# Kernel optimization log

Measured on AMD Instinct MI355X. Metric: run time of the kernel, lower is better.

## Reference

```python
import jax, jax.numpy as jnp
import numpy as np

D_MODEL = 64
D_STATE = 16
D_CONV = 4
EXPAND = 2
D_INNER = EXPAND * D_MODEL        # 128
DT_RANK = max(1, D_MODEL // 16)   # 4 (mamba_ssm default ceil(d_model/16))
BATCH, HH, WW = 2, 128, 128


def setup_inputs() -> dict:
    key = jax.random.key(0)
    ks = jax.random.split(key, 10)
    def norm(k, shape, sc=0.05):
        return jax.random.normal(k, shape, jnp.float32) * sc
    # A initialized as in mamba_ssm: A = 1..d_state per channel, stored as log
    A_log = jnp.log(jnp.tile(jnp.arange(1, D_STATE + 1, dtype=jnp.float32), (4, D_INNER, 1)))
    return {
        "x": jax.random.normal(ks[0], (BATCH, D_MODEL, HH, WW), jnp.float32),
        "in_w": norm(ks[1], (4, 2 * D_INNER, D_MODEL)),
        "conv_w": norm(ks[2], (4, D_INNER, D_CONV), 0.2),
        "conv_b": jnp.zeros((4, D_INNER), jnp.float32),
        "xp_w": norm(ks[3], (4, DT_RANK + 2 * D_STATE, D_INNER)),
        "dtp_w": norm(ks[4], (4, D_INNER, DT_RANK), 0.2),
        "dtp_b": jnp.full((4, D_INNER), -4.0, jnp.float32) + norm(ks[5], (4, D_INNER), 0.5),
        "A_log": A_log,
        "Dp": jnp.ones((4, D_INNER), jnp.float32),
        "out_w": norm(ks[6], (4, D_MODEL, D_INNER)),
        "fuse_w": norm(ks[7], (D_MODEL, 4 * D_MODEL)),
        "fuse_b": jnp.zeros((D_MODEL,), jnp.float32),
        "ln_g": jnp.ones((D_MODEL,), jnp.float32),
        "ln_b": jnp.zeros((D_MODEL,), jnp.float32),
    }


def _mamba(xseq, in_w, conv_w, conv_b, xp_w, dtp_w, dtp_b, A_log, Dp, out_w):
    # xseq: (N, L, d_model) -> (N, L, d_model). Single-direction Mamba block.
    N, L, _ = xseq.shape
    xz = xseq @ in_w.T                       # (N, L, 2*d_inner)
    u, z = jnp.split(xz, 2, axis=-1)
    # causal depthwise conv1d, kernel width D_CONV
    up = jnp.pad(u, ((0, 0), (D_CONV - 1, 0), (0, 0)))
    uc = conv_b + sum(up[:, k:k + L, :] * conv_w[:, k][None, None, :] for k in range(D_CONV))
    uc = jax.nn.silu(uc)
    dbl = uc @ xp_w.T                        # (N, L, dt_rank + 2*d_state)
    dt = jax.nn.softplus(dbl[..., :DT_RANK] @ dtp_w.T + dtp_b)   # (N, L, d_inner)
    Bm = dbl[..., DT_RANK:DT_RANK + D_STATE]                     # (N, L, d_state)
    Cm = dbl[..., DT_RANK + D_STATE:]                            # (N, L, d_state)
    A = -jnp.exp(A_log)                                          # (d_inner, d_state)

    def step(h, inp):
        dt_t, B_t, C_t, u_t = inp            # (N,d_inner),(N,d_state),(N,d_state),(N,d_inner)
        h = h * jnp.exp(dt_t[..., None] * A) + (dt_t * u_t)[..., None] * B_t[:, None, :]
        y = jnp.einsum('nds,ns->nd', h, C_t)
        return h, y

    h0 = jnp.zeros((N, D_INNER, D_STATE), xseq.dtype)
    _, ys = jax.lax.scan(step, h0, (dt.swapaxes(0, 1), Bm.swapaxes(0, 1),
                                    Cm.swapaxes(0, 1), uc.swapaxes(0, 1)))
    y = ys.swapaxes(0, 1) + uc * Dp
    y = y * jax.nn.silu(z)
    return y @ out_w.T


def reference(x, in_w, conv_w, conv_b, xp_w, dtp_w, dtp_b, A_log, Dp, out_w,
              fuse_w, fuse_b, ln_g, ln_b):
    B, C, H, W = x.shape
    xhwc = x.transpose(0, 2, 3, 1)           # (B,H,W,C)
    xwhc = x.transpose(0, 3, 2, 1)           # (B,W,H,C)
    d0 = xhwc.reshape(B * H, W, C)                         # horizontal fwd
    d1 = xhwc[:, :, ::-1, :].reshape(B * H, W, C)          # horizontal bwd
    d2 = xwhc.reshape(B * W, H, C)                         # vertical fwd
    d3 = xwhc[:, :, ::-1, :].reshape(B * W, H, C)          # vertical bwd
    xd = jnp.stack([d0, d1, d2, d3])         # (4, B*S, S, C) since H == W
    ys = jax.vmap(_mamba)(xd, in_w, conv_w, conv_b, xp_w, dtp_w, dtp_b, A_log, Dp, out_w)
    y0 = ys[0].reshape(B, H, W, C)
    y1 = ys[1].reshape(B, H, W, C)[:, :, ::-1, :]
    y2 = ys[2].reshape(B, W, H, C).transpose(0, 2, 1, 3)
    y3 = ys[3].reshape(B, W, H, C)[:, :, ::-1, :].transpose(0, 2, 1, 3)
    cat = jnp.concatenate([y0, y1, y2, y3], axis=-1)       # (B,H,W,4C)
    f = cat @ fuse_w.T + fuse_b                            # 1x1 conv
    mu = f.mean(-1, keepdims=True)
    var = f.var(-1, keepdims=True)
    f = (f - mu) * jax.lax.rsqrt(var + 1e-5) * ln_g + ln_b # LayerNorm over C
    f = jax.nn.silu(f)
    return f.transpose(0, 3, 1, 2)                          # (B,C,H,W)
```

## Files before the change

### kernel.cpp

```cpp
#include <hip/hip_runtime.h>
#include <hip/hip_bf16.h>
#include <math.h>


typedef __attribute__((ext_vector_type(8))) short short8;
typedef __attribute__((ext_vector_type(4))) float f32x4;
typedef __attribute__((ext_vector_type(2))) float f32x2;

__device__ __forceinline__ f32x2 pk_mul(f32x2 a, f32x2 b) {
  f32x2 d;
  asm("v_pk_mul_f32 %0, %1, %2" : "=v"(d) : "v"(a), "v"(b));
  return d;
}
__device__ __forceinline__ f32x2 pk_fma(f32x2 a, f32x2 b, f32x2 c) {
  f32x2 d;
  asm("v_pk_fma_f32 %0, %1, %2, %3" : "=v"(d) : "v"(a), "v"(b), "v"(c));
  return d;
}

__device__ __forceinline__ unsigned int pk2bf(float a, float b) {
  __hip_bfloat162 h = __float22bfloat162_rn(make_float2(a, b));
  unsigned int u;
  __builtin_memcpy(&u, &h, 4);
  return u;
}
__device__ __forceinline__ unsigned short f2bf(float f) {
  __hip_bfloat16 h = __float2bfloat16(f);
  unsigned short s;
  __builtin_memcpy(&s, &h, 2);
  return s;
}
__device__ __forceinline__ float bf2f(unsigned short h) {
  return __uint_as_float(((unsigned int)h) << 16);
}
__device__ __forceinline__ float fastrcp(float x) { return __builtin_amdgcn_rcpf(x); }
__device__ __forceinline__ float siluf(float x) { return x * fastrcp(1.f + __expf(-x)); }

__global__ void k0_prep(const float* __restrict__ out_w, const float* __restrict__ fuse_w,
                        const float* __restrict__ in_w, const float* __restrict__ xp_w,
                        const float* __restrict__ x,
                        unsigned short* __restrict__ MT16, unsigned short* __restrict__ W16,
                        unsigned short* __restrict__ XW16, unsigned short* __restrict__ XH,
                        unsigned short* __restrict__ XW) {
  __shared__ unsigned short sT[64*132];
  int blk = blockIdx.x;
  int tid = threadIdx.x;
  if (blk < 128) {
    int idx = blk * 256 + tid;
    int d   = idx & 127;
    int o   = (idx >> 7) & 63;
    int dir = idx >> 13;
    float acc = 0.f;
    #pragma unroll 8
    for (int j = 0; j < 64; ++j)
      acc += out_w[(dir*64 + j)*128 + d] * fuse_w[o*256 + dir*64 + j];
    MT16[o*512 + dir*128 + d] = f2bf(acc);
  } else if (blk < 160) {
    int t = (blk - 128) * 256 + tid;
    int base = t * 8;
    float4 v0 = *(const float4*)(in_w + base);
    float4 v1 = *(const float4*)(in_w + base + 4);
    uint4 pk;
    pk.x = pk2bf(v0.x, v0.y);
    pk.y = pk2bf(v0.z, v0.w);
    pk.z = pk2bf(v1.x, v1.y);
    pk.w = pk2bf(v1.z, v1.w);
    *(uint4*)(W16 + base) = pk;
  } else if (blk < 164) {
    int t = (blk - 160) * 256 + tid;
    for (int pid = t; pid < 4*48*128; pid += 1024) {
      int dir = pid / 6144;
      int rem = pid - dir*6144;
      int row = rem >> 7, c = rem & 127;
      XW16[pid] = (row < 36) ? f2bf(xp_w[dir*4608 + row*128 + c]) : (unsigned short)0;
    }
  } else {
    int idx = blk - 164;
    int b = idx >> 7, h = idx & 127;
    for (int f = tid*4; f < 8192; f += 1024) {
      int c = f >> 7, w = f & 127;
      float4 v = *(const float4*)(x + (((size_t)(b*64 + c)*128 + h)*128 + w));
      sT[c*132 + w + 0] = f2bf(v.x);
      sT[c*132 + w + 1] = f2bf(v.y);
      sT[c*132 + w + 2] = f2bf(v.z);
      sT[c*132 + w + 3] = f2bf(v.w);
    }
    __syncthreads();
    for (int f = tid*8; f < 8192; f += 2048) {
      int w = f >> 6, c0 = f & 63;
      unsigned int pk[4];
      #pragma unroll
      for (int p = 0; p < 4; ++p) {
        unsigned int lo = sT[(c0 + p*2 + 0)*132 + w];
        unsigned int hi = sT[(c0 + p*2 + 1)*132 + w];
        pk[p] = lo | (hi << 16);
      }
      uint4 v; v.x = pk[0]; v.y = pk[1]; v.z = pk[2]; v.w = pk[3];
      *(uint4*)(XH + (((size_t)(b*128 + h)*128 + w)*64 + c0)) = v;
      *(uint4*)(XW + (((size_t)(b*128 + w)*128 + h)*64 + c0)) = v;
    }
  }
}

__global__ __launch_bounds__(256, 3) void k1_front(
    const unsigned short* __restrict__ XH, const unsigned short* __restrict__ XW,
    const unsigned short* __restrict__ W16, const unsigned short* __restrict__ XW16,
    const float* __restrict__ conv_w, const float* __restrict__ conv_b,
    const float* __restrict__ dtp_w, const float* __restrict__ dtp_b,
    const float* __restrict__ A_log, const float* __restrict__ Dp,
    unsigned short* __restrict__ YF)
{
  __shared__ __align__(16) char smem[53248];
  float* sBCf         = (float*)smem;
  unsigned short* sUC = (unsigned short*)(smem + 18432);

  const int tid = threadIdx.x;
  const int dir = blockIdx.x >> 8;
  const int n   = blockIdx.x & 255;
  const int b   = n >> 7;
  const int r   = n & 127;
  const int n_all = dir*256 + n;

  const unsigned short* xsrc = (dir < 2 ? XH : XW) + ((size_t)(b*128 + r)*128)*64;

  const int wave = tid >> 6;
  const int lane = tid & 63;
  const int m16 = lane & 15;
  const int quad = lane >> 4;
  const int tb0 = wave * 32;
  const int st0 = tb0 + m16;
  const int st1 = tb0 + 16 + m16;
  const int sp0 = (dir & 1) ? (127 - st0) : st0;
  const int sp1 = (dir & 1) ? (127 - st1) : st1;

  unsigned int zpk[2][8][2];

  {
    short8 bfr[2][2];
    #pragma unroll
    for (int ks = 0; ks < 2; ++ks) {
      bfr[0][ks] = *(const short8*)(xsrc + sp0*64 + ks*32 + quad*8);
      bfr[1][ks] = *(const short8*)(xsrc + sp1*64 + ks*32 + quad*8);
    }
    const unsigned short* Wd = W16 + (size_t)dir * 16384;

    for (int rt = 0; rt < 8; ++rt) {
      short8 af[2];
      #pragma unroll
      for (int ks = 0; ks < 2; ++ks)
        af[ks] = *(const short8*)(Wd + (rt*16 + m16)*64 + ks*32 + quad*8);
      #pragma unroll
      for (int tt = 0; tt < 2; ++tt) {
        f32x4 acc = {0.f, 0.f, 0.f, 0.f};
        acc = __builtin_amdgcn_mfma_f32_16x16x32_bf16(af[0], bfr[tt][0], acc, 0, 0, 0);
        acc = __builtin_amdgcn_mfma_f32_16x16x32_bf16(af[1], bfr[tt][1], acc, 0, 0, 0);
        const int tok = tt ? st1 : st0;
        const int r0 = rt*16 + quad*4;
        uint2 u2;
        u2.x = pk2bf(acc[0], acc[1]);
        u2.y = pk2bf(acc[2], acc[3]);
        *(uint2*)(sUC + tok*136 + r0) = u2;
      }
    }
    #pragma unroll
    for (int k = 0; k < 8; ++k) {
      short8 af[2];
      #pragma unroll
      for (int ks = 0; ks < 2; ++ks)
        af[ks] = *(const short8*)(Wd + ((8+k)*16 + m16)*64 + ks*32 + quad*8);
      #pragma unroll
      for (int tt = 0; tt < 2; ++tt) {
        f32x4 acc = {0.f, 0.f, 0.f, 0.f};
        acc = __builtin_amdgcn_mfma_f32_16x16x32_bf16(af[0], bfr[tt][0], acc, 0, 0, 0);
        acc = __builtin_amdgcn_mfma_f32_16x16x32_bf16(af[1], bfr[tt][1], acc, 0, 0, 0);
        zpk[tt][k][0] = pk2bf(siluf(acc[0]), siluf(acc[1]));
        zpk[tt][k][1] = pk2bf(siluf(acc[2]), siluf(acc[3]));
      }
    }
  }
  __syncthreads();

  {
    const int d = tid & 127;
    const int half = tid >> 7;
    const int ca = half * 32;
    const int cb2 = (half + 2) * 32;
    const float* cw = conv_w + (size_t)(dir*128 + d)*4;
    const float c0w = cw[0], c1w = cw[1], c2w = cw[2], c3w = cw[3];
    const float cbv = conv_b[dir*128 + d];
    const f32x2 cw0v = {c0w, c0w}, cw1v = {c1w, c1w}, cw2v = {c2w, c2w}, cw3v = {c3w, c3w};
    const f32x2 cbv2 = {cbv, cbv};
    f32x2 A0 = { half ? bf2f(sUC[(ca-3)*136 + d]) : 0.f, bf2f(sUC[(cb2-3)*136 + d]) };
    f32x2 A1 = { half ? bf2f(sUC[(ca-2)*136 + d]) : 0.f, bf2f(sUC[(cb2-2)*136 + d]) };
    f32x2 A2 = { half ? bf2f(sUC[(ca-1)*136 + d]) : 0.f, bf2f(sUC[(cb2-1)*136 + d]) };
    __syncthreads();
    unsigned short* pa = sUC + ca*136 + d;
    unsigned short* pb = sUC + cb2*136 + d;
    for (int i = 0; i < 32; ++i) {
      f32x2 cur = { bf2f(*pa), bf2f(*pb) };
      f32x2 v = pk_fma(cw3v, cur,
                pk_fma(cw2v, A2,
                pk_fma(cw1v, A1,
                pk_fma(cw0v, A0, cbv2))));
      *pa = f2bf(siluf(v.x));
      *pb = f2bf(siluf(v.y));
      A0 = A1; A1 = A2; A2 = cur;
      pa += 136; pb += 136;
    }
  }
  __syncthreads();

  {
    short8 bfr[2][4];
    #pragma unroll
    for (int tt = 0; tt < 2; ++tt)
      #pragma unroll
      for (int ks = 0; ks < 4; ++ks)
        bfr[tt][ks] = *(const short8*)(sUC + (tt ? st1 : st0)*136 + ks*32 + quad*8);

    const unsigned short* XWd = XW16 + (size_t)dir * (48*128);

    for (int rt = 0; rt < 3; ++rt) {
      short8 af[4];
      #pragma unroll
      for (int ks = 0; ks < 4; ++ks)
        af[ks] = *(const short8*)(XWd + (rt*16 + m16)*128 + ks*32 + quad*8);
      #pragma unroll
      for (int tt = 0; tt < 2; ++tt) {
        f32x4 acc = {0.f, 0.f, 0.f, 0.f};
        #pragma unroll
        for (int ks = 0; ks < 4; ++ks)
          acc = __builtin_amdgcn_mfma_f32_16x16x32_bf16(af[ks], bfr[tt][ks], acc, 0, 0, 0);
        const int tok = tt ? st1 : st0;
        const int r0 = rt*16 + quad*4;
        if (r0 == 0) {
          float4 v; v.x = acc[0]; v.y = acc[1]; v.z = acc[2]; v.w = acc[3];
          *(float4*)(smem + 18432 + tok*272 + 256) = v;
        } else if (r0 < 36) {
          float4 v; v.x = acc[0]; v.y = acc[1]; v.z = acc[2]; v.w = acc[3];
          *(float4*)(sBCf + tok*36 + (r0 - 4)) = v;
        }
      }
    }
  }
  __syncthreads();

  {
    const int d = tid >> 1;
    const int p = tid & 1;
    const float* dwp = dtp_w + (size_t)(dir*128 + d) * 4;
    const float dw0 = dwp[0], dw1 = dwp[1], dw2 = dwp[2], dw3 = dwp[3];
    const float db = dtp_b[dir*128 + d];
    const float dpv = Dp[dir*128 + d];

    float Av[8];
    bool fast = true;
    #pragma unroll
    for (int j = 0; j < 8; ++j) {
      float a = -__expf(A_log[((size_t)(dir*128 + d))*16 + p*8 + j]);
      Av[j] = a;
      if (fabsf((-a) - (float)(p*8 + j + 1)) > 1e-3f) fast = false;
    }

    if (fast) {
      f32x2 h0 = {0.f, 0.f}, h1 = {0.f, 0.f}, h2v = {0.f, 0.f}, h3 = {0.f, 0.f};
      const char* qp = smem + 18432 + 256;
      const float* bp = sBCf + p*8;
      const float* cp = sBCf + 16 + p*8;
      const unsigned short* up = sUC + d;
      unsigned short* yo = sUC + d;
      for (int l = 0; l < 128; ++l) {
        float4 Q = *(const float4*)qp;
        f32x2 B01 = *(const f32x2*)(bp + 0), B23 = *(const f32x2*)(bp + 2);
        f32x2 B45 = *(const f32x2*)(bp + 4), B67 = *(const f32x2*)(bp + 6);
        f32x2 C01 = *(const f32x2*)(cp + 0), C23 = *(const f32x2*)(cp + 2);
        f32x2 C45 = *(const f32x2*)(cp + 4), C67 = *(const f32x2*)(cp + 6);
        float u = bf2f(*up);
        float dr = Q.x*dw0 + Q.y*dw1 + Q.z*dw2 + Q.w*dw3 + db;
        float te = __expf(dr);
        float dt = (dr > 20.f) ? dr : __logf(1.f + te);
        float dtu = dt * u;
        float E = fastrcp(1.f + te);
        float E2 = E*E, E4 = E2*E2, E8 = E4*E4;
        float eb = p ? E8 : 1.f;
        f32x2 P0 = {E*eb, E2*eb};
        f32x2 E2v = {E2, E2};
        f32x2 P1 = pk_mul(P0, E2v);
        f32x2 P2 = pk_mul(P1, E2v);
        f32x2 P3 = pk_mul(P2, E2v);
        f32x2 du = {dtu, dtu};
        h0  = pk_fma(h0,  P0, pk_mul(du, B01));
        h1  = pk_fma(h1,  P1, pk_mul(du, B23));
        h2v = pk_fma(h2v, P2, pk_mul(du, B45));
        h3  = pk_fma(h3,  P3, pk_mul(du, B67));
        f32x2 ya = pk_mul(h0, C01);
        f32x2 yb = pk_mul(h1, C23);
        ya = pk_fma(h2v, C45, ya);
        yb = pk_fma(h3,  C67, yb);
        float ypar = (ya.x + ya.y) + (yb.x + yb.y);
        float ot = __uint_as_float((unsigned int)__builtin_amdgcn_mov_dpp(
                     (int)__float_as_uint(ypar), 0xB1, 0xF, 0xF, true));
        float ysum = ypar + ot;
        *yo = f2bf(ysum + u*dpv);
        qp += 272; bp += 36; cp += 36; up += 136; yo += 136;
      }
    } else {
      float h[8];
      #pragma unroll
      for (int j = 0; j < 8; ++j) h[j] = 0.f;
      for (int l = 0; l < 128; ++l) {
        float4 Q = *(const float4*)(smem + 18432 + l*272 + 256);
        float4 b0 = *(const float4*)(sBCf + l*36 + p*8);
        float4 b1 = *(const float4*)(sBCf + l*36 + p*8 + 4);
        float4 c0 = *(const float4*)(sBCf + l*36 + 16 + p*8);
        float4 c1 = *(const float4*)(sBCf + l*36 + 16 + p*8 + 4);
        float Bv[8] = {b0.x,b0.y,b0.z,b0.w, b1.x,b1.y,b1.z,b1.w};
        float Cv[8] = {c0.x,c0.y,c0.z,c0.w, c1.x,c1.y,c1.z,c1.w};
        float u = bf2f(sUC[l*136 + d]);
        float dr = Q.x*dw0 + Q.y*dw1 + Q.z*dw2 + Q.w*dw3 + db;
        float te = __expf(dr);
        float dt = (dr > 20.f) ? dr : __logf(1.f + te);
        float dtu = dt * u;
        float yp = 0.f;
        #pragma unroll
        for (int j = 0; j < 8; ++j) {
          float ej = __expf(dt*Av[j]);
          h[j] = h[j]*ej + dtu*Bv[j];
          yp += h[j]*Cv[j];
        }
        float ot = __uint_as_float((unsigned int)__builtin_amdgcn_mov_dpp(
                     (int)__float_as_uint(yp), 0xB1, 0xF, 0xF, true));
        float ysum = yp + ot;
        if (p == 0) sUC[l*136 + d] = f2bf(ysum + u*dpv);
      }
    }
  }
  __syncthreads();

  #pragma unroll
  for (int tt = 0; tt < 2; ++tt) {
    const int st = tt ? st1 : st0;
    size_t rowbase;
    if (dir < 2)       rowbase = ((size_t)n_all*128 + st)*128;
    else if (dir == 2) rowbase = ((size_t)(512 + b*128 + st)*128 + r)*128;
    else               rowbase = ((size_t)(768 + b*128 + (127-st))*128 + r)*128;
    #pragma unroll
    for (int k = 0; k < 8; ++k) {
      const int dz = 16*k + quad*4;
      uint2 yv = *(const uint2*)(sUC + st*136 + dz);
      float y0 = __uint_as_float(yv.x << 16);
      float y1 = __uint_as_float(yv.x & 0xffff0000u);
      float y2 = __uint_as_float(yv.y << 16);
      float y3 = __uint_as_float(yv.y & 0xffff0000u);
      unsigned int z01 = zpk[tt][k][0], z23 = zpk[tt][k][1];
      float z0 = __uint_as_float(z01 << 16);
      float z1 = __uint_as_float(z01 & 0xffff0000u);
      float z2 = __uint_as_float(z23 << 16);
      float z3 = __uint_as_float(z23 & 0xffff0000u);
      uint2 ov;
      ov.x = pk2bf(y0*z0, y1*z1);
      ov.y = pk2bf(y2*z2, y3*z3);
      *(uint2*)(YF + rowbase + dz) = ov;
    }
  }
}

__global__ __launch_bounds__(256, 2) void k3_fuse(
    const unsigned short* __restrict__ YF, const unsigned short* __restrict__ MT16,
    const float* __restrict__ fuse_b, const float* __restrict__ ln_g,
    const float* __restrict__ ln_b, float* __restrict__ out)
{
  __shared__ __align__(16) unsigned short sYB[64*520];

  const int tid = threadIdx.x;
  const int blk = blockIdx.x;
  const int b = blk >> 8;
  const int rr2 = blk & 255;
  const int h = rr2 >> 1;
  const int w0 = (rr2 & 1) * 64;

  for (int f = tid*8; f < 32768; f += 2048) {
    int dirg = f >> 13;
    int rem = f & 8191;
    int tok = rem >> 7;
    int dd = rem & 127;
    int X = (dirg == 1) ? (127 - w0 - tok) : (w0 + tok);
    size_t base = ((size_t)(dirg*256 + b*128 + h)*128 + X)*128 + dd;
    *(uint4*)(sYB + tok*520 + dirg*128 + dd) = *(const uint4*)(YF + base);
  }
  __syncthreads();

  const int wave = tid >> 6;
  const int lane = tid & 63;
  const int m16 = lane & 15;
  const int quad = lane >> 4;
  const int tok = wave*16 + m16;

  short8 bfr[16];
  #pragma unroll
  for (int jt = 0; jt < 16; ++jt)
    bfr[jt] = *(const short8*)(sYB + tok*520 + jt*32 + quad*8);

  float facc[4][4];
  #pragma unroll
  for (int mt = 0; mt < 4; ++mt) {
    f32x4 acc = {0.f, 0.f, 0.f, 0.f};
    #pragma unroll
    for (int jt = 0; jt < 16; ++jt) {
      short8 af = *(const short8*)(MT16 + (size_t)(mt*16 + m16)*512 + jt*32 + quad*8);
      acc = __builtin_amdgcn_mfma_f32_16x16x32_bf16(af, bfr[jt], acc, 0, 0, 0);
    }
    facc[mt][0] = acc[0]; facc[mt][1] = acc[1]; facc[mt][2] = acc[2]; facc[mt][3] = acc[3];
  }

  float fv[16];
  float s1 = 0.f, s2 = 0.f;
  #pragma unroll
  for (int mt = 0; mt < 4; ++mt)
    #pragma unroll
    for (int rr = 0; rr < 4; ++rr) {
      int o = mt*16 + quad*4 + rr;
      float v = facc[mt][rr] + fuse_b[o];
      fv[mt*4 + rr] = v;
      s1 += v; s2 += v*v;
    }
  s1 += __shfl_xor(s1, 16, 64); s1 += __shfl_xor(s1, 32, 64);
  s2 += __shfl_xor(s2, 16, 64); s2 += __shfl_xor(s2, 32, 64);
  float mu = s1 * (1.f/64.f);
  float var = s2 * (1.f/64.f) - mu*mu;
  float rs = rsqrtf(var + 1e-5f);

  #pragma unroll
  for (int mt = 0; mt < 4; ++mt)
    #pragma unroll
    for (int rr = 0; rr < 4; ++rr) {
      int o = mt*16 + quad*4 + rr;
      float v = (fv[mt*4 + rr] - mu) * rs * ln_g[o] + ln_b[o];
      out[((size_t)(b*64 + o)*128 + h)*128 + (w0 + tok)] = siluf(v);
    }
}

extern "C" void kernel_launch(void* const* d_in, const int* in_sizes, int n_in,
                              void* d_out, int out_size, void* d_ws, size_t ws_size,
                              hipStream_t stream) {
  const float* x      = (const float*)d_in[0];
  const float* in_w   = (const float*)d_in[1];
  const float* conv_w = (const float*)d_in[2];
  const float* conv_b = (const float*)d_in[3];
  const float* xp_w   = (const float*)d_in[4];
  const float* dtp_w  = (const float*)d_in[5];
  const float* dtp_b  = (const float*)d_in[6];
  const float* A_log  = (const float*)d_in[7];
  const float* Dp     = (const float*)d_in[8];
  const float* out_w  = (const float*)d_in[9];
  const float* fuse_w = (const float*)d_in[10];
  const float* fuse_b = (const float*)d_in[11];
  const float* ln_g   = (const float*)d_in[12];
  const float* ln_b   = (const float*)d_in[13];
  float* out = (float*)d_out;

  char* ws = (char*)d_ws;
  unsigned short* YF   = (unsigned short*)(ws);
  unsigned short* MT16 = (unsigned short*)(ws + 33554432);
  unsigned short* W16  = (unsigned short*)(ws + 33619968);
  unsigned short* XW16 = (unsigned short*)(ws + 33751040);
  unsigned short* XH   = (unsigned short*)(ws + 33800192);
  unsigned short* XWt  = (unsigned short*)(ws + 37994496);

  k0_prep<<<dim3(420), dim3(256), 0, stream>>>(out_w, fuse_w, in_w, xp_w, x,
                                               MT16, W16, XW16, XH, XWt);
  k1_front<<<dim3(1024), dim3(256), 0, stream>>>(XH, XWt, W16, XW16, conv_w, conv_b,
                                                 dtp_w, dtp_b, A_log, Dp, YF);
  k3_fuse<<<dim3(512), dim3(256), 0, stream>>>(YF, MT16, fuse_b, ln_g, ln_b, out);
}
```

Before: 205.0 us.

## Split front kernel into projection/conv kernel and separate global-memory scan kernel

After: 272.8 us. 33.0% more time.

```diff
diff --git a/kernel.cpp b/kernel.cpp
--- a/kernel.cpp
+++ b/kernel.cpp
@@ -102,17 +102,14 @@
   }
 }
 
-__global__ __launch_bounds__(256, 3) void k1_front(
+__global__ __launch_bounds__(256, 4) void k1a_front(
     const unsigned short* __restrict__ XH, const unsigned short* __restrict__ XW,
     const unsigned short* __restrict__ W16, const unsigned short* __restrict__ XW16,
     const float* __restrict__ conv_w, const float* __restrict__ conv_b,
-    const float* __restrict__ dtp_w, const float* __restrict__ dtp_b,
-    const float* __restrict__ A_log, const float* __restrict__ Dp,
-    unsigned short* __restrict__ YF)
+    unsigned short* __restrict__ UCg, unsigned short* __restrict__ ZFg,
+    float* __restrict__ BCg)
 {
-  __shared__ __align__(16) char smem[53248];
-  float* sBCf         = (float*)smem;
-  unsigned short* sUC = (unsigned short*)(smem + 18432);
+  __shared__ __align__(16) unsigned short sUC[128*136];
 
   const int tid = threadIdx.x;
   const int dir = blockIdx.x >> 8;
@@ -132,8 +129,6 @@
   const int st1 = tb0 + 16 + m16;
   const int sp0 = (dir & 1) ? (127 - st0) : st0;
   const int sp1 = (dir & 1) ? (127 - st1) : st1;
-
-  unsigned int zpk[2][8][2];
 
   {
     short8 bfr[2][2];
@@ -162,6 +157,7 @@
         *(uint2*)(sUC + tok*136 + r0) = u2;
       }
     }
+    unsigned short* zn = ZFg + (size_t)n_all * 16384;
     #pragma unroll
     for (int k = 0; k < 8; ++k) {
       short8 af[2];
@@ -173,8 +169,11 @@
         f32x4 acc = {0.f, 0.f, 0.f, 0.f};
         acc = __builtin_amdgcn_mfma_f32_16x16x32_bf16(af[0], bfr[tt][0], acc, 0, 0, 0);
         acc = __builtin_amdgcn_mfma_f32_16x16x32_bf16(af[1], bfr[tt][1], acc, 0, 0, 0);
-        zpk[tt][k][0] = pk2bf(siluf(acc[0]), siluf(acc[1]));
-        zpk[tt][k][1] = pk2bf(siluf(acc[2]), siluf(acc[3]));
+        const int tok = tt ? st1 : st0;
+        uint2 zv;
+        zv.x = pk2bf(siluf(acc[0]), siluf(acc[1]));
+        zv.y = pk2bf(siluf(acc[2]), siluf(acc[3]));
+        *(uint2*)(zn + tok*128 + 16*k + quad*4) = zv;
       }
     }
   }
@@ -211,6 +210,14 @@
   __syncthreads();
 
   {
+    unsigned short* ucn = UCg + (size_t)n_all * 16384;
+    #pragma unroll
+    for (int c = 0; c < 8; ++c) {
+      int idx = tid + c*256;
+      int tok = idx >> 4, u4 = idx & 15;
+      *(uint4*)(ucn + tok*128 + u4*8) = *(const uint4*)(sUC + tok*136 + u4*8);
+    }
+
     short8 bfr[2][4];
     #pragma unroll
     for (int tt = 0; tt < 2; ++tt)
@@ -219,6 +226,7 @@
         bfr[tt][ks] = *(const short8*)(sUC + (tt ? st1 : st0)*136 + ks*32 + quad*8);
 
     const unsigned short* XWd = XW16 + (size_t)dir * (48*128);
+    float* bcn = BCg + (size_t)n_all * 4608;
 
     for (int rt = 0; rt < 3; ++rt) {
       short8 af[4];
@@ -232,135 +240,146 @@
         for (int ks = 0; ks < 4; ++ks)
           acc = __builtin_amdgcn_mfma_f32_16x16x32_bf16(af[ks], bfr[tt][ks], acc, 0, 0, 0);
         const int tok = tt ? st1 : st0;
-        const int r0 = rt*16 + quad*4;
-        if (r0 == 0) {
+        const int g = rt*4 + quad;
+        if (g < 9) {
           float4 v; v.x = acc[0]; v.y = acc[1]; v.z = acc[2]; v.w = acc[3];
-          *(float4*)(smem + 18432 + tok*272 + 256) = v;
-        } else if (r0 < 36) {
-          float4 v; v.x = acc[0]; v.y = acc[1]; v.z = acc[2]; v.w = acc[3];
-          *(float4*)(sBCf + tok*36 + (r0 - 4)) = v;
+          *(float4*)(bcn + g*512 + tok*4) = v;
         }
       }
     }
   }
-  __syncthreads();
-
-  {
-    const int d = tid >> 1;
-    const int p = tid & 1;
-    const float* dwp = dtp_w + (size_t)(dir*128 + d) * 4;
-    const float dw0 = dwp[0], dw1 = dwp[1], dw2 = dwp[2], dw3 = dwp[3];
-    const float db = dtp_b[dir*128 + d];
-    const float dpv = Dp[dir*128 + d];
-
-    float Av[8];
-    bool fast = true;
-    #pragma unroll
-    for (int j = 0; j < 8; ++j) {
-      float a = -__expf(A_log[((size_t)(dir*128 + d))*16 + p*8 + j]);
-      Av[j] = a;
-      if (fabsf((-a) - (float)(p*8 + j + 1)) > 1e-3f) fast = false;
-    }
-
-    if (fast) {
-      f32x2 h0 = {0.f, 0.f}, h1 = {0.f, 0.f}, h2v = {0.f, 0.f}, h3 = {0.f, 0.f};
-      const char* qp = smem + 18432 + 256;
-      const float* bp = sBCf + p*8;
-      const float* cp = sBCf + 16 + p*8;
-      const unsigned short* up = sUC + d;
-      unsigned short* yo = sUC + d;
-      for (int l = 0; l < 128; ++l) {
-        float4 Q = *(const float4*)qp;
-        f32x2 B01 = *(const f32x2*)(bp + 0), B23 = *(const f32x2*)(bp + 2);
-        f32x2 B45 = *(const f32x2*)(bp + 4), B67 = *(const f32x2*)(bp + 6);
-        f32x2 C01 = *(const f32x2*)(cp + 0), C23 = *(const f32x2*)(cp + 2);
-        f32x2 C45 = *(const f32x2*)(cp + 4), C67 = *(const f32x2*)(cp + 6);
-        float u = bf2f(*up);
-        float dr = Q.x*dw0 + Q.y*dw1 + Q.z*dw2 + Q.w*dw3 + db;
-        float te = __expf(dr);
-        float dt = (dr > 20.f) ? dr : __logf(1.f + te);
-        float dtu = dt * u;
-        float E = fastrcp(1.f + te);
-        float E2 = E*E, E4 = E2*E2, E8 = E4*E4;
-        float eb = p ? E8 : 1.f;
-        f32x2 P0 = {E*eb, E2*eb};
-        f32x2 E2v = {E2, E2};
-        f32x2 P1 = pk_mul(P0, E2v);
-        f32x2 P2 = pk_mul(P1, E2v);
-        f32x2 P3 = pk_mul(P2, E2v);
-        f32x2 du = {dtu, dtu};
-        h0  = pk_fma(h0,  P0, pk_mul(du, B01));
-        h1  = pk_fma(h1,  P1, pk_mul(du, B23));
-        h2v = pk_fma(h2v, P2, pk_mul(du, B45));
-        h3  = pk_fma(h3,  P3, pk_mul(du, B67));
-        f32x2 ya = pk_mul(h0, C01);
-        f32x2 yb = pk_mul(h1, C23);
-        ya = pk_fma(h2v, C45, ya);
-        yb = pk_fma(h3,  C67, yb);
-        float ypar = (ya.x + ya.y) + (yb.x + yb.y);
-        float ot = __uint_as_float((unsigned int)__builtin_amdgcn_mov_dpp(
-                     (int)__float_as_uint(ypar), 0xB1, 0xF, 0xF, true));
-        float ysum = ypar + ot;
-        *yo = f2bf(ysum + u*dpv);
-        qp += 272; bp += 36; cp += 36; up += 136; yo += 136;
+}
+
+__global__ __launch_bounds__(256, 4) void k1b_scan(
+    const unsigned short* __restrict__ UCg, const unsigned short* __restrict__ ZFg,
+    const float* __restrict__ BCg,
+    const float* __restrict__ dtp_w, const float* __restrict__ dtp_b,
+    const float* __restrict__ A_log, const float* __restrict__ Dp,
+    unsigned short* __restrict__ YF)
+{
+  const int tid = threadIdx.x;
+  const int dir = blockIdx.x >> 8;
+  const int n   = blockIdx.x & 255;
+  const int b   = n >> 7;
+  const int r   = n & 127;
+  const int n_all = dir*256 + n;
+  const int d = tid >> 1;
+  const int p = tid & 1;
+
+  const float* dwp = dtp_w + (size_t)(dir*128 + d) * 4;
+  const float dw0 = dwp[0], dw1 = dwp[1], dw2 = dwp[2], dw3 = dwp[3];
+  const float db = dtp_b[dir*128 + d];
+  const float dpv = Dp[dir*128 + d];
+
+  float Av[8];
+  bool fast = true;
+  #pragma unroll
+  for (int j = 0; j < 8; ++j) {
+    float a = -__expf(A_log[((size_t)(dir*128 + d))*16 + p*8 + j]);
+    Av[j] = a;
+    if (fabsf((-a) - (float)(p*8 + j + 1)) > 1e-3f) fast = false;
+  }
+
+  const float* bcn = BCg + (size_t)n_all * 4608;
+  const float* qp  = bcn;
+  const float* bp0 = bcn + (1 + 2*p)*512;
+  const float* bp1 = bcn + (2 + 2*p)*512;
+  const float* cp0 = bcn + (5 + 2*p)*512;
+  const float* cp1 = bcn + (6 + 2*p)*512;
+  const unsigned short* up = UCg + (size_t)n_all*16384 + d;
+  const unsigned short* zp = ZFg + (size_t)n_all*16384 + d;
+
+  unsigned short* yo;
+  long ystep;
+  if (dir < 2) {
+    yo = YF + ((size_t)n_all*128)*128 + d;                       ystep = 128;
+  } else if (dir == 2) {
+    yo = YF + ((size_t)((512 + b*128)*128 + r))*128 + d;         ystep = 16384;
+  } else {
+    yo = YF + ((size_t)((768 + b*128 + 127)*128 + r))*128 + d;   ystep = -16384;
+  }
+
+  if (fast) {
+    f32x2 h0 = {0.f,0.f}, h1 = {0.f,0.f}, h2v = {0.f,0.f}, h3 = {0.f,0.f};
+    float4 Q   = *(const float4*)(qp);
+    float4 Bq0 = *(const float4*)(bp0), Bq1 = *(const float4*)(bp1);
+    float4 Cq0 = *(const float4*)(cp0), Cq1 = *(const float4*)(cp1);
+    float u  = bf2f(*up);
+    float zf = bf2f(*zp);
+    for (int l = 0; l < 128; ++l) {
+      const int a4   = (l < 127) ? 4 : 0;
+      const int a128 = (l < 127) ? 128 : 0;
+      float4 Qn  = *(const float4*)(qp  + a4);
+      float4 Bn0 = *(const float4*)(bp0 + a4);
+      float4 Bn1 = *(const float4*)(bp1 + a4);
+      float4 Cn0 = *(const float4*)(cp0 + a4);
+      float4 Cn1 = *(const float4*)(cp1 + a4);
+      float un   = bf2f(up[a128]);
+      float zn   = bf2f(zp[a128]);
+
+      float dr = Q.x*dw0 + Q.y*dw1 + Q.z*dw2 + Q.w*dw3 + db;
+      float te = __expf(dr);
+      float dt = (dr > 20.f) ? dr : __logf(1.f + te);
+      float dtu = dt * u;
+      float E = fastrcp(1.f + te);
+      float E2 = E*E, E4 = E2*E2, E8 = E4*E4;
+      float eb = p ? E8 : 1.f;
+      f32x2 P0 = {E*eb, E2*eb};
+      f32x2 E2v = {E2, E2};
+      f32x2 P1 = pk_mul(P0, E2v);
+      f32x2 P2 = pk_mul(P1, E2v);
+      f32x2 P3 = pk_mul(P2, E2v);
+      f32x2 du = {dtu, dtu};
+      f32x2 B01 = {Bq0.x,Bq0.y}, B23 = {Bq0.z,Bq0.w};
+      f32x2 B45 = {Bq1.x,Bq1.y}, B67 = {Bq1.z,Bq1.w};
+      f32x2 C01 = {Cq0.x,Cq0.y}, C23 = {Cq0.z,Cq0.w};
+      f32x2 C45 = {Cq1.x,Cq1.y}, C67 = {Cq1.z,Cq1.w};
+      h0  = pk_fma(h0,  P0, pk_mul(du, B01));
+      h1  = pk_fma(h1,  P1, pk_mul(du, B23));
+      h2v = pk_fma(h2v, P2, pk_mul(du, B45));
+      h3  = pk_fma(h3,  P3, pk_mul(du, B67));
+      f32x2 ya = pk_mul(h0, C01);
+      f32x2 yb = pk_mul(h1, C23);
+      ya = pk_fma(h2v, C45, ya);
+      yb = pk_fma(h3,  C67, yb);
+      float ypar = (ya.x + ya.y) + (yb.x + yb.y);
+      float ot = __uint_as_float((unsigned int)__builtin_amdgcn_mov_dpp(
+                   (int)__float_as_uint(ypar), 0xB1, 0xF, 0xF, true));
+      float ysum = ypar + ot;
+      *yo = f2bf((ysum + u*dpv) * zf);
+      yo += ystep;
+      qp += 4; bp0 += 4; bp1 += 4; cp0 += 4; cp1 += 4; up += 128; zp += 128;
+      Q = Qn; Bq0 = Bn0; Bq1 = Bn1; Cq0 = Cn0; Cq1 = Cn1; u = un; zf = zn;
+    }
+  } else {
+    float h[8];
+    #pragma unroll
+    for (int j = 0; j < 8; ++j) h[j] = 0.f;
+    for (int l = 0; l < 128; ++l) {
+      float4 Q   = *(const float4*)(qp);
+      float4 Bq0 = *(const float4*)(bp0), Bq1 = *(const float4*)(bp1);
+      float4 Cq0 = *(const float4*)(cp0), Cq1 = *(const float4*)(cp1);
+      float Bv[8] = {Bq0.x,Bq0.y,Bq0.z,Bq0.w, Bq1.x,Bq1.y,Bq1.z,Bq1.w};
+      float Cv[8] = {Cq0.x,Cq0.y,Cq0.z,Cq0.w, Cq1.x,Cq1.y,Cq1.z,Cq1.w};
+      float u  = bf2f(*up);
+      float zf = bf2f(*zp);
+      float dr = Q.x*dw0 + Q.y*dw1 + Q.z*dw2 + Q.w*dw3 + db;
+      float te = __expf(dr);
+      float dt = (dr > 20.f) ? dr : __logf(1.f + te);
+      float dtu = dt * u;
+      float yp = 0.f;
+      #pragma unroll
+      for (int j = 0; j < 8; ++j) {
+        float ej = __expf(dt*Av[j]);
+        h[j] = h[j]*ej + dtu*Bv[j];
+        yp += h[j]*Cv[j];
       }
-    } else {
-      float h[8];
-      #pragma unroll
-      for (int j = 0; j < 8; ++j) h[j] = 0.f;
-      for (int l = 0; l < 128; ++l) {
-        float4 Q = *(const float4*)(smem + 18432 + l*272 + 256);
-        float4 b0 = *(const float4*)(sBCf + l*36 + p*8);
-        float4 b1 = *(const float4*)(sBCf + l*36 + p*8 + 4);
-        float4 c0 = *(const float4*)(sBCf + l*36 + 16 + p*8);
-        float4 c1 = *(const float4*)(sBCf + l*36 + 16 + p*8 + 4);
-        float Bv[8] = {b0.x,b0.y,b0.z,b0.w, b1.x,b1.y,b1.z,b1.w};
-        float Cv[8] = {c0.x,c0.y,c0.z,c0.w, c1.x,c1.y,c1.z,c1.w};
-        float u = bf2f(sUC[l*136 + d]);
-        float dr = Q.x*dw0 + Q.y*dw1 + Q.z*dw2 + Q.w*dw3 + db;
-        float te = __expf(dr);
-        float dt = (dr > 20.f) ? dr : __logf(1.f + te);
-        float dtu = dt * u;
-        float yp = 0.f;
-        #pragma unroll
-        for (int j = 0; j < 8; ++j) {
-          float ej = __expf(dt*Av[j]);
-          h[j] = h[j]*ej + dtu*Bv[j];
-          yp += h[j]*Cv[j];
-        }
-        float ot = __uint_as_float((unsigned int)__builtin_amdgcn_mov_dpp(
-                     (int)__float_as_uint(yp), 0xB1, 0xF, 0xF, true));
-        float ysum = yp + ot;
-        if (p == 0) sUC[l*136 + d] = f2bf(ysum + u*dpv);
-      }
-    }
-  }
-  __syncthreads();
-
-  #pragma unroll
-  for (int tt = 0; tt < 2; ++tt) {
-    const int st = tt ? st1 : st0;
-    size_t rowbase;
-    if (dir < 2)       rowbase = ((size_t)n_all*128 + st)*128;
-    else if (dir == 2) rowbase = ((size_t)(512 + b*128 + st)*128 + r)*128;
-    else               rowbase = ((size_t)(768 + b*128 + (127-st))*128 + r)*128;
-    #pragma unroll
-    for (int k = 0; k < 8; ++k) {
-      const int dz = 16*k + quad*4;
-      uint2 yv = *(const uint2*)(sUC + st*136 + dz);
-      float y0 = __uint_as_float(yv.x << 16);
-      float y1 = __uint_as_float(yv.x & 0xffff0000u);
-      float y2 = __uint_as_float(yv.y << 16);
-      float y3 = __uint_as_float(yv.y & 0xffff0000u);
-      unsigned int z01 = zpk[tt][k][0], z23 = zpk[tt][k][1];
-      float z0 = __uint_as_float(z01 << 16);
-      float z1 = __uint_as_float(z01 & 0xffff0000u);
-      float z2 = __uint_as_float(z23 << 16);
-      float z3 = __uint_as_float(z23 & 0xffff0000u);
-      uint2 ov;
-      ov.x = pk2bf(y0*z0, y1*z1);
-      ov.y = pk2bf(y2*z2, y3*z3);
-      *(uint2*)(YF + rowbase + dz) = ov;
+      float ot = __uint_as_float((unsigned int)__builtin_amdgcn_mov_dpp(
+                   (int)__float_as_uint(yp), 0xB1, 0xF, 0xF, true));
+      float ysum = yp + ot;
+      *yo = f2bf((ysum + u*dpv) * zf);
+      yo += ystep;
+      qp += 4; bp0 += 4; bp1 += 4; cp0 += 4; cp1 += 4; up += 128; zp += 128;
     }
   }
 }
@@ -466,10 +485,15 @@
   unsigned short* XW16 = (unsigned short*)(ws + 33751040);
   unsigned short* XH   = (unsigned short*)(ws + 33800192);
   unsigned short* XWt  = (unsigned short*)(ws + 37994496);
+  unsigned short* UCg  = (unsigned short*)(ws + 42188800);
+  unsigned short* ZFg  = (unsigned short*)(ws + 75743232);
+  float*          BCg  = (float*)(ws + 109297664);
 
   k0_prep<<<dim3(420), dim3(256), 0, stream>>>(out_w, fuse_w, in_w, xp_w, x,
                                                MT16, W16, XW16, XH, XWt);
-  k1_front<<<dim3(1024), dim3(256), 0, stream>>>(XH, XWt, W16, XW16, conv_w, conv_b,
-                                                 dtp_w, dtp_b, A_log, Dp, YF);
+  k1a_front<<<dim3(1024), dim3(256), 0, stream>>>(XH, XWt, W16, XW16, conv_w, conv_b,
+                                                  UCg, ZFg, BCg);
+  k1b_scan<<<dim3(1024), dim3(256), 0, stream>>>(UCg, ZFg, BCg, dtp_w, dtp_b,
+                                                 A_log, Dp, YF);
   k3_fuse<<<dim3(512), dim3(256), 0, stream>>>(YF, MT16, fuse_b, ln_g, ln_b, out);
 }
```

## Double k1_front block to 512 threads, splitting tokens and SSM states across more lanes

Applied to the files above, without the earlier changes.

Result: slower. 248.3 us (+21.1%).

```diff
diff --git a/kernel.cpp b/kernel.cpp
--- a/kernel.cpp
+++ b/kernel.cpp
@@ -102,7 +102,7 @@
   }
 }
 
-__global__ __launch_bounds__(256, 3) void k1_front(
+__global__ __launch_bounds__(512, 2) void k1_front(
     const unsigned short* __restrict__ XH, const unsigned short* __restrict__ XW,
     const unsigned short* __restrict__ W16, const unsigned short* __restrict__ XW16,
     const float* __restrict__ conv_w, const float* __restrict__ conv_b,
@@ -110,7 +110,7 @@
     const float* __restrict__ A_log, const float* __restrict__ Dp,
     unsigned short* __restrict__ YF)
 {
-  __shared__ __align__(16) char smem[53248];
+  __shared__ __align__(16) char smem[55296];
   float* sBCf         = (float*)smem;
   unsigned short* sUC = (unsigned short*)(smem + 18432);
 
@@ -127,21 +127,16 @@
   const int lane = tid & 63;
   const int m16 = lane & 15;
   const int quad = lane >> 4;
-  const int tb0 = wave * 32;
-  const int st0 = tb0 + m16;
-  const int st1 = tb0 + 16 + m16;
-  const int sp0 = (dir & 1) ? (127 - st0) : st0;
-  const int sp1 = (dir & 1) ? (127 - st1) : st1;
-
-  unsigned int zpk[2][8][2];
+  const int st = wave*16 + m16;
+  const int sp = (dir & 1) ? (127 - st) : st;
+
+  unsigned int zpk[8][2];
 
   {
-    short8 bfr[2][2];
-    #pragma unroll
-    for (int ks = 0; ks < 2; ++ks) {
-      bfr[0][ks] = *(const short8*)(xsrc + sp0*64 + ks*32 + quad*8);
-      bfr[1][ks] = *(const short8*)(xsrc + sp1*64 + ks*32 + quad*8);
-    }
+    short8 bfr[2];
+    #pragma unroll
+    for (int ks = 0; ks < 2; ++ks)
+      bfr[ks] = *(const short8*)(xsrc + sp*64 + ks*32 + quad*8);
     const unsigned short* Wd = W16 + (size_t)dir * 16384;
 
     for (int rt = 0; rt < 8; ++rt) {
@@ -149,18 +144,14 @@
       #pragma unroll
       for (int ks = 0; ks < 2; ++ks)
         af[ks] = *(const short8*)(Wd + (rt*16 + m16)*64 + ks*32 + quad*8);
-      #pragma unroll
-      for (int tt = 0; tt < 2; ++tt) {
-        f32x4 acc = {0.f, 0.f, 0.f, 0.f};
-        acc = __builtin_amdgcn_mfma_f32_16x16x32_bf16(af[0], bfr[tt][0], acc, 0, 0, 0);
-        acc = __builtin_amdgcn_mfma_f32_16x16x32_bf16(af[1], bfr[tt][1], acc, 0, 0, 0);
-        const int tok = tt ? st1 : st0;
-        const int r0 = rt*16 + quad*4;
-        uint2 u2;
-        u2.x = pk2bf(acc[0], acc[1]);
-        u2.y = pk2bf(acc[2], acc[3]);
-        *(uint2*)(sUC + tok*136 + r0) = u2;
-      }
+      f32x4 acc = {0.f, 0.f, 0.f, 0.f};
+      acc = __builtin_amdgcn_mfma_f32_16x16x32_bf16(af[0], bfr[0], acc, 0, 0, 0);
+      acc = __builtin_amdgcn_mfma_f32_16x16x32_bf16(af[1], bfr[1], acc, 0, 0, 0);
+      const int r0 = rt*16 + quad*4;
+      uint2 u2;
+      u2.x = pk2bf(acc[0], acc[1]);
+      u2.y = pk2bf(acc[2], acc[3]);
+      *(uint2*)(sUC + st*136 + r0) = u2;
     }
     #pragma unroll
     for (int k = 0; k < 8; ++k) {
@@ -168,55 +159,42 @@
       #pragma unroll
       for (int ks = 0; ks < 2; ++ks)
         af[ks] = *(const short8*)(Wd + ((8+k)*16 + m16)*64 + ks*32 + quad*8);
-      #pragma unroll
-      for (int tt = 0; tt < 2; ++tt) {
-        f32x4 acc = {0.f, 0.f, 0.f, 0.f};
-        acc = __builtin_amdgcn_mfma_f32_16x16x32_bf16(af[0], bfr[tt][0], acc, 0, 0, 0);
-        acc = __builtin_amdgcn_mfma_f32_16x16x32_bf16(af[1], bfr[tt][1], acc, 0, 0, 0);
-        zpk[tt][k][0] = pk2bf(siluf(acc[0]), siluf(acc[1]));
-        zpk[tt][k][1] = pk2bf(siluf(acc[2]), siluf(acc[3]));
-      }
+      f32x4 acc = {0.f, 0.f, 0.f, 0.f};
+      acc = __builtin_amdgcn_mfma_f32_16x16x32_bf16(af[0], bfr[0], acc, 0, 0, 0);
+      acc = __builtin_amdgcn_mfma_f32_16x16x32_bf16(af[1], bfr[1], acc, 0, 0, 0);
+      zpk[k][0] = pk2bf(siluf(acc[0]), siluf(acc[1]));
+      zpk[k][1] = pk2bf(siluf(acc[2]), siluf(acc[3]));
     }
   }
   __syncthreads();
 
   {
     const int d = tid & 127;
-    const int half = tid >> 7;
-    const int ca = half * 32;
-    const int cb2 = (half + 2) * 32;
+    const int c = tid >> 7;
+    const int ca = c * 32;
     const float* cw = conv_w + (size_t)(dir*128 + d)*4;
     const float c0w = cw[0], c1w = cw[1], c2w = cw[2], c3w = cw[3];
     const float cbv = conv_b[dir*128 + d];
-    const f32x2 cw0v = {c0w, c0w}, cw1v = {c1w, c1w}, cw2v = {c2w, c2w}, cw3v = {c3w, c3w};
-    const f32x2 cbv2 = {cbv, cbv};
-    f32x2 A0 = { half ? bf2f(sUC[(ca-3)*136 + d]) : 0.f, bf2f(sUC[(cb2-3)*136 + d]) };
-    f32x2 A1 = { half ? bf2f(sUC[(ca-2)*136 + d]) : 0.f, bf2f(sUC[(cb2-2)*136 + d]) };
-    f32x2 A2 = { half ? bf2f(sUC[(ca-1)*136 + d]) : 0.f, bf2f(sUC[(cb2-1)*136 + d]) };
+    float a0 = c ? bf2f(sUC[(ca-3)*136 + d]) : 0.f;
+    float a1 = c ? bf2f(sUC[(ca-2)*136 + d]) : 0.f;
+    float a2 = c ? bf2f(sUC[(ca-1)*136 + d]) : 0.f;
     __syncthreads();
     unsigned short* pa = sUC + ca*136 + d;
-    unsigned short* pb = sUC + cb2*136 + d;
     for (int i = 0; i < 32; ++i) {
-      f32x2 cur = { bf2f(*pa), bf2f(*pb) };
-      f32x2 v = pk_fma(cw3v, cur,
-                pk_fma(cw2v, A2,
-                pk_fma(cw1v, A1,
-                pk_fma(cw0v, A0, cbv2))));
-      *pa = f2bf(siluf(v.x));
-      *pb = f2bf(siluf(v.y));
-      A0 = A1; A1 = A2; A2 = cur;
-      pa += 136; pb += 136;
+      float cur = bf2f(*pa);
+      float v = cbv + c0w*a0 + c1w*a1 + c2w*a2 + c3w*cur;
+      *pa = f2bf(siluf(v));
+      a0 = a1; a1 = a2; a2 = cur;
+      pa += 136;
     }
   }
   __syncthreads();
 
   {
-    short8 bfr[2][4];
-    #pragma unroll
-    for (int tt = 0; tt < 2; ++tt)
-      #pragma unroll
-      for (int ks = 0; ks < 4; ++ks)
-        bfr[tt][ks] = *(const short8*)(sUC + (tt ? st1 : st0)*136 + ks*32 + quad*8);
+    short8 bfr[4];
+    #pragma unroll
+    for (int ks = 0; ks < 4; ++ks)
+      bfr[ks] = *(const short8*)(sUC + st*136 + ks*32 + quad*8);
 
     const unsigned short* XWd = XW16 + (size_t)dir * (48*128);
 
@@ -225,56 +203,50 @@
       #pragma unroll
       for (int ks = 0; ks < 4; ++ks)
         af[ks] = *(const short8*)(XWd + (rt*16 + m16)*128 + ks*32 + quad*8);
-      #pragma unroll
-      for (int tt = 0; tt < 2; ++tt) {
-        f32x4 acc = {0.f, 0.f, 0.f, 0.f};
-        #pragma unroll
-        for (int ks = 0; ks < 4; ++ks)
-          acc = __builtin_amdgcn_mfma_f32_16x16x32_bf16(af[ks], bfr[tt][ks], acc, 0, 0, 0);
-        const int tok = tt ? st1 : st0;
-        const int r0 = rt*16 + quad*4;
-        if (r0 == 0) {
-          float4 v; v.x = acc[0]; v.y = acc[1]; v.z = acc[2]; v.w = acc[3];
-          *(float4*)(smem + 18432 + tok*272 + 256) = v;
-        } else if (r0 < 36) {
-          float4 v; v.x = acc[0]; v.y = acc[1]; v.z = acc[2]; v.w = acc[3];
-          *(float4*)(sBCf + tok*36 + (r0 - 4)) = v;
-        }
+      f32x4 acc = {0.f, 0.f, 0.f, 0.f};
+      #pragma unroll
+      for (int ks = 0; ks < 4; ++ks)
+        acc = __builtin_amdgcn_mfma_f32_16x16x32_bf16(af[ks], bfr[ks], acc, 0, 0, 0);
+      const int r0 = rt*16 + quad*4;
+      if (r0 == 0) {
+        float4 v; v.x = acc[0]; v.y = acc[1]; v.z = acc[2]; v.w = acc[3];
+        *(float4*)(smem + 18432 + st*272 + 256) = v;
+      } else if (r0 < 36) {
+        float4 v; v.x = acc[0]; v.y = acc[1]; v.z = acc[2]; v.w = acc[3];
+        *(float4*)(sBCf + st*36 + (r0 - 4)) = v;
       }
     }
   }
   __syncthreads();
 
   {
-    const int d = tid >> 1;
-    const int p = tid & 1;
+    const int d = tid >> 2;
+    const int p = tid & 3;
     const float* dwp = dtp_w + (size_t)(dir*128 + d) * 4;
     const float dw0 = dwp[0], dw1 = dwp[1], dw2 = dwp[2], dw3 = dwp[3];
     const float db = dtp_b[dir*128 + d];
     const float dpv = Dp[dir*128 + d];
 
-    float Av[8];
+    float Av[4];
     bool fast = true;
     #pragma unroll
-    for (int j = 0; j < 8; ++j) {
-      float a = -__expf(A_log[((size_t)(dir*128 + d))*16 + p*8 + j]);
+    for (int j = 0; j < 4; ++j) {
+      float a = -__expf(A_log[((size_t)(dir*128 + d))*16 + p*4 + j]);
       Av[j] = a;
-      if (fabsf((-a) - (float)(p*8 + j + 1)) > 1e-3f) fast = false;
+      if (fabsf((-a) - (float)(p*4 + j + 1)) > 1e-3f) fast = false;
     }
 
     if (fast) {
-      f32x2 h0 = {0.f, 0.f}, h1 = {0.f, 0.f}, h2v = {0.f, 0.f}, h3 = {0.f, 0.f};
+      f32x2 h0 = {0.f, 0.f}, h1 = {0.f, 0.f};
       const char* qp = smem + 18432 + 256;
-      const float* bp = sBCf + p*8;
-      const float* cp = sBCf + 16 + p*8;
+      const float* bp = sBCf + p*4;
+      const float* cp = sBCf + 16 + p*4;
       const unsigned short* up = sUC + d;
       unsigned short* yo = sUC + d;
       for (int l = 0; l < 128; ++l) {
-        float4 Q = *(const float4*)qp;
-        f32x2 B01 = *(const f32x2*)(bp + 0), B23 = *(const f32x2*)(bp + 2);
-        f32x2 B45 = *(const f32x2*)(bp + 4), B67 = *(const f32x2*)(bp + 6);
-        f32x2 C01 = *(const f32x2*)(cp + 0), C23 = *(const f32x2*)(cp + 2);
-        f32x2 C45 = *(const f32x2*)(cp + 4), C67 = *(const f32x2*)(cp + 6);
+        float4 Q  = *(const float4*)qp;
+        float4 Bq = *(const float4*)bp;
+        float4 Cq = *(const float4*)cp;
         float u = bf2f(*up);
         float dr = Q.x*dw0 + Q.y*dw1 + Q.z*dw2 + Q.w*dw3 + db;
         float te = __expf(dr);
@@ -282,40 +254,41 @@
         float dtu = dt * u;
         float E = fastrcp(1.f + te);
         float E2 = E*E, E4 = E2*E2, E8 = E4*E4;
-        float eb = p ? E8 : 1.f;
-        f32x2 P0 = {E*eb, E2*eb};
+        float m1 = (p & 1) ? E4 : 1.f;
+        float m2 = (p & 2) ? E8 : 1.f;
+        float eb = m1 * m2;
+        f32x2 Ee = {E, E2};
+        f32x2 ebv = {eb, eb};
+        f32x2 P0 = pk_mul(Ee, ebv);
         f32x2 E2v = {E2, E2};
         f32x2 P1 = pk_mul(P0, E2v);
-        f32x2 P2 = pk_mul(P1, E2v);
-        f32x2 P3 = pk_mul(P2, E2v);
         f32x2 du = {dtu, dtu};
-        h0  = pk_fma(h0,  P0, pk_mul(du, B01));
-        h1  = pk_fma(h1,  P1, pk_mul(du, B23));
-        h2v = pk_fma(h2v, P2, pk_mul(du, B45));
-        h3  = pk_fma(h3,  P3, pk_mul(du, B67));
+        f32x2 B01 = {Bq.x, Bq.y}, B23 = {Bq.z, Bq.w};
+        f32x2 C01 = {Cq.x, Cq.y}, C23 = {Cq.z, Cq.w};
+        h0 = pk_fma(h0, P0, pk_mul(du, B01));
+        h1 = pk_fma(h1, P1, pk_mul(du, B23));
         f32x2 ya = pk_mul(h0, C01);
-        f32x2 yb = pk_mul(h1, C23);
-        ya = pk_fma(h2v, C45, ya);
-        yb = pk_fma(h3,  C67, yb);
-        float ypar = (ya.x + ya.y) + (yb.x + yb.y);
-        float ot = __uint_as_float((unsigned int)__builtin_amdgcn_mov_dpp(
+        ya = pk_fma(h1, C23, ya);
+        float ypar = ya.x + ya.y;
+        float t1 = __uint_as_float((unsigned int)__builtin_amdgcn_mov_dpp(
                      (int)__float_as_uint(ypar), 0xB1, 0xF, 0xF, true));
-        float ysum = ypar + ot;
+        float s1 = ypar + t1;
+        float t2 = __uint_as_float((unsigned int)__builtin_amdgcn_mov_dpp(
+                     (int)__float_as_uint(s1), 0x4E, 0xF, 0xF, true));
+        float ysum = s1 + t2;
         *yo = f2bf(ysum + u*dpv);
         qp += 272; bp += 36; cp += 36; up += 136; yo += 136;
       }
     } else {
-      float h[8];
-      #pragma unroll
-      for (int j = 0; j < 8; ++j) h[j] = 0.f;
+      float h[4];
+      #pragma unroll
+      for (int j = 0; j < 4; ++j) h[j] = 0.f;
       for (int l = 0; l < 128; ++l) {
-        float4 Q = *(const float4*)(smem + 18432 + l*272 + 256);
-        float4 b0 = *(const float4*)(sBCf + l*36 + p*8);
-        float4 b1 = *(const float4*)(sBCf + l*36 + p*8 + 4);
-        float4 c0 = *(const float4*)(sBCf + l*36 + 16 + p*8);
-        float4 c1 = *(const float4*)(sBCf + l*36 + 16 + p*8 + 4);
-        float Bv[8] = {b0.x,b0.y,b0.z,b0.w, b1.x,b1.y,b1.z,b1.w};
-        float Cv[8] = {c0.x,c0.y,c0.z,c0.w, c1.x,c1.y,c1.z,c1.w};
+        float4 Q  = *(const float4*)(smem + 18432 + l*272 + 256);
+        float4 Bq = *(const float4*)(sBCf + l*36 + p*4);
+        float4 Cq = *(const float4*)(sBCf + l*36 + 16 + p*4);
+        float Bv[4] = {Bq.x, Bq.y, Bq.z, Bq.w};
+        float Cv[4] = {Cq.x, Cq.y, Cq.z, Cq.w};
         float u = bf2f(sUC[l*136 + d]);
         float dr = Q.x*dw0 + Q.y*dw1 + Q.z*dw2 + Q.w*dw3 + db;
         float te = __expf(dr);
@@ -323,23 +296,25 @@
         float dtu = dt * u;
         float yp = 0.f;
         #pragma unroll
-        for (int j = 0; j < 8; ++j) {
+        for (int j = 0; j < 4; ++j) {
           float ej = __expf(dt*Av[j]);
           h[j] = h[j]*ej + dtu*Bv[j];
           yp += h[j]*Cv[j];
         }
-        float ot = __uint_as_float((unsigned int)__builtin_amdgcn_mov_dpp(
+        float t1 = __uint_as_float((unsigned int)__builtin_amdgcn_mov_dpp(
                      (int)__float_as_uint(yp), 0xB1, 0xF, 0xF, true));
-        float ysum = yp + ot;
-        if (p == 0) sUC[l*136 + d] = f2bf(ysum + u*dpv);
+        float s1 = yp + t1;
+        float t2 = __uint_as_float((unsigned int)__builtin_amdgcn_mov_dpp(
+                     (int)__float_as_uint(s1), 0x4E, 0xF, 0xF, true));
+        float ysum = s1 + t2;
+        *(sUC + l*136 + d) = f2bf(ysum + u*dpv);
+        (void)0;
       }
     }
   }
   __syncthreads();
 
-  #pragma unroll
-  for (int tt = 0; tt < 2; ++tt) {
-    const int st = tt ? st1 : st0;
+  {
     size_t rowbase;
     if (dir < 2)       rowbase = ((size_t)n_all*128 + st)*128;
     else if (dir == 2) rowbase = ((size_t)(512 + b*128 + st)*128 + r)*128;
@@ -352,7 +327,7 @@
       float y1 = __uint_as_float(yv.x & 0xffff0000u);
       float y2 = __uint_as_float(yv.y << 16);
       float y3 = __uint_as_float(yv.y & 0xffff0000u);
-      unsigned int z01 = zpk[tt][k][0], z23 = zpk[tt][k][1];
+      unsigned int z01 = zpk[k][0], z23 = zpk[k][1];
       float z0 = __uint_as_float(z01 << 16);
       float z1 = __uint_as_float(z01 & 0xffff0000u);
       float z2 = __uint_as_float(z23 << 16);
@@ -469,7 +444,7 @@
 
   k0_prep<<<dim3(420), dim3(256), 0, stream>>>(out_w, fuse_w, in_w, xp_w, x,
                                                MT16, W16, XW16, XH, XWt);
-  k1_front<<<dim3(1024), dim3(256), 0, stream>>>(XH, XWt, W16, XW16, conv_w, conv_b,
+  k1_front<<<dim3(1024), dim3(512), 0, stream>>>(XH, XWt, W16, XW16, conv_w, conv_b,
                                                  dtp_w, dtp_b, A_log, Dp, YF);
   k3_fuse<<<dim3(512), dim3(256), 0, stream>>>(YF, MT16, fuse_b, ln_g, ln_b, out);
 }
```
